# Kernel optimization log

Measured on AMD Instinct MI355X. Metric: run time of the kernel, lower is better.

## Reference

```python
import jax, jax.numpy as jnp
import numpy as np
import math

D_MODEL = 1024
D_STATE = 16
D_CONV = 4
EXPAND = 2
D_INNER = EXPAND * D_MODEL  # 2048
DT_RANK = 64
B_SZ = 2
L_SEQ = 1024


def setup_inputs() -> dict:
    key = jax.random.key(0)
    ks = jax.random.split(key, 10)
    x = jax.random.normal(ks[0], (B_SZ, L_SEQ, D_MODEL), dtype=jnp.float32)
    in_proj_w = jax.random.normal(ks[1], (2 * D_INNER, D_MODEL), dtype=jnp.float32) * (1.0 / math.sqrt(D_MODEL))
    conv_w = jax.random.normal(ks[2], (D_INNER, 1, D_CONV), dtype=jnp.float32) * (1.0 / math.sqrt(D_CONV))
    conv_b = jax.random.normal(ks[3], (D_INNER,), dtype=jnp.float32) * 0.01
    x_proj_w = jax.random.normal(ks[4], (DT_RANK + 2 * D_STATE, D_INNER), dtype=jnp.float32) * (1.0 / math.sqrt(D_INNER))
    dt_init_std = DT_RANK ** (-0.5)
    dt_proj_w = jax.random.uniform(ks[5], (D_INNER, DT_RANK), dtype=jnp.float32, minval=-dt_init_std, maxval=dt_init_std)
    dt = jnp.exp(jax.random.uniform(ks[6], (D_INNER,), dtype=jnp.float32) * (math.log(0.1) - math.log(0.001)) + math.log(0.001))
    dt = jnp.clip(dt, 1e-4, None)
    dt_proj_b = dt + jnp.log(-jnp.expm1(-dt))
    A_log = jnp.log(jnp.tile(jnp.arange(1, D_STATE + 1, dtype=jnp.float32)[None, :], (D_INNER, 1)))
    D = jnp.ones((D_INNER,), dtype=jnp.float32)
    out_proj_w = jax.random.normal(ks[7], (D_MODEL, D_INNER), dtype=jnp.float32) * (1.0 / math.sqrt(D_INNER))
    return {"x": x, "in_proj_w": in_proj_w, "conv_w": conv_w, "conv_b": conv_b,
            "x_proj_w": x_proj_w, "dt_proj_w": dt_proj_w, "dt_proj_b": dt_proj_b,
            "A_log": A_log, "D": D, "out_proj_w": out_proj_w}


def _mamba_forward(x, in_proj_w, conv_w, conv_b, x_proj_w, dt_proj_w, dt_proj_b, A_log, D, out_proj_w):
    B, L, _ = x.shape
    # input projection -> x, z each [B, L, Di]
    xz = jnp.einsum('bld,ed->ble', x, in_proj_w)
    xs, z = jnp.split(xz, 2, axis=-1)
    # causal depthwise conv along L (torch pads K-1 both sides then trims -> left pad only)
    xc = jnp.transpose(xs, (0, 2, 1))  # [B, Di, L]
    xc = jax.lax.conv_general_dilated(
        xc, conv_w, window_strides=(1,), padding=[(D_CONV - 1, 0)],
        feature_group_count=D_INNER, dimension_numbers=('NCH', 'OIH', 'NCH'))
    xc = xc + conv_b[None, :, None]
    xs = jnp.transpose(xc, (0, 2, 1))  # [B, L, Di]
    xs = jax.nn.silu(xs)
    # SSM parameters
    A = -jnp.exp(A_log)  # [Di, N]
    dbc = jnp.einsum('bld,ed->ble', xs, x_proj_w)
    delta_r = dbc[..., :DT_RANK]
    Bm = dbc[..., DT_RANK:DT_RANK + D_STATE]       # [B, L, N]
    Cm = dbc[..., DT_RANK + D_STATE:]              # [B, L, N]
    delta = jnp.einsum('blr,dr->bld', delta_r, dt_proj_w)
    delta = jax.nn.softplus(delta + dt_proj_b)     # [B, L, Di]
    # selective scan: h_t = exp(delta*A)*h_{t-1} + delta*B*x
    dA = jnp.exp(delta[..., None] * A)                          # [B, L, Di, N]
    dBx = (delta * xs)[..., None] * Bm[:, :, None, :]           # [B, L, Di, N]
    dA_t = jnp.moveaxis(dA, 1, 0)    # [L, B, Di, N]
    dBx_t = jnp.moveaxis(dBx, 1, 0)
    C_t = jnp.moveaxis(Cm, 1, 0)     # [L, B, N]
    h0 = jnp.zeros((B, D_INNER, D_STATE), dtype=xs.dtype)

    def step(h, inp):
        da, bx, c = inp
        h = da * h + bx
        y = jnp.einsum('bdn,bn->bd', h, c)
        return h, y

    _, ys = jax.lax.scan(step, h0, (dA_t, dBx_t, C_t))
    y = jnp.moveaxis(ys, 0, 1)       # [B, L, Di]
    y = y + D * xs
    # gating and output projection
    out = y * jax.nn.silu(z)
    return jnp.einsum('bld,od->blo', out, out_proj_w)


def reference(x, in_proj_w, conv_w, conv_b, x_proj_w, dt_proj_w, dt_proj_b, A_log, D, out_proj_w):
    return _mamba_forward(x, in_proj_w, conv_w, conv_b, x_proj_w, dt_proj_w, dt_proj_b, A_log, D, out_proj_w)
```

## Files before the change

kernel.cpp:

```cpp
#include <hip/hip_runtime.h>
#include <hip/hip_bf16.h>

typedef __attribute__((ext_vector_type(8))) short short8;
typedef __attribute__((ext_vector_type(4))) float f32x4;
typedef __hip_bfloat16 bf16;

#define D_MODEL 1024
#define D_INNER 2048
#define DT_RANK 64
#define D_STATE 16
#define B_SZ 2
#define L_SEQ 1024
#define NSEG 64
#define SL 16

__device__ __forceinline__ float b2f(bf16 x){ return __bfloat162float(x); }
__device__ __forceinline__ bf16  f2b(float x){ return __float2bfloat16(x); }

__device__ __forceinline__ void cvt_store8(bf16* dst, const float* s){
  union { short8 v; bf16 e[8]; } u;
  #pragma unroll
  for (int i = 0; i < 8; i++) u.e[i] = f2b(s[i]);
  *(short8*)dst = u.v;
}

__device__ __forceinline__ void gl_lds16(const bf16* g, bf16* l){
  __builtin_amdgcn_global_load_lds((const __attribute__((address_space(1))) unsigned int*)g,
                                   (__attribute__((address_space(3))) unsigned int*)l, 16, 0, 0);
}

__global__ __launch_bounds__(256) void cvt5_k(const float* s0, bf16* d0, int c0,
                                              const float* s1, bf16* d1, int c1,
                                              const float* s2, bf16* d2, int c2,
                                              const float* s3, bf16* d3, int c3,
                                              const float* s4, bf16* d4, int c4)
{
  int i = blockIdx.x * 256 + threadIdx.x;
  const float* s; bf16* d; int off;
  if      (i < c0) { s = s0; d = d0; off = i; }
  else if (i < c1) { s = s1; d = d1; off = i - c0; }
  else if (i < c2) { s = s2; d = d2; off = i - c1; }
  else if (i < c3) { s = s3; d = d3; off = i - c2; }
  else if (i < c4) { s = s4; d = d4; off = i - c3; }
  else return;
  float b[8];
  *(float4*)&b[0] = *(const float4*)(s + (size_t)off * 8);
  *(float4*)&b[4] = *(const float4*)(s + (size_t)off * 8 + 4);
  cvt_store8(d + (size_t)off * 8, b);
}

template<int MODE, int JT>
__global__ __launch_bounds__(256) void gemm_glds(const bf16* __restrict__ A,
                                                 const bf16* __restrict__ B,
                                                 void* __restrict__ Cout,
                                                 const float* __restrict__ bias,
                                                 int M, int N, int K)
{
  constexpr int BN = JT * 32;
  constexpr int BI = BN / 64;
  __shared__ bf16 As[128 * 32];
  __shared__ bf16 Bs[BN * 32];
  const int bm = blockIdx.y * 128, bn = blockIdx.x * BN;
  const int tid  = threadIdx.x;
  const int lane = tid & 63, wave = tid >> 6;
  const int wm = (wave & 1) * 64, wn = (wave >> 1) * (JT * 16);
  const int r = lane & 15, q = lane >> 4;

  const bf16* asrc[2];
  #pragma unroll
  for (int i = 0; i < 2; i++) {
    int c = i * 256 + tid;
    asrc[i] = A + (size_t)(bm + (c >> 2)) * K + (c & 3) * 8;
  }
  const bf16* bsrc[BI];
  #pragma unroll
  for (int i = 0; i < BI; i++) {
    int c = i * 256 + tid;
    bsrc[i] = B + (size_t)(bn + (c >> 2)) * K + (c & 3) * 8;
  }

  f32x4 acc[4][JT];
  #pragma unroll
  for (int i = 0; i < 4; i++)
    #pragma unroll
    for (int j = 0; j < JT; j++) acc[i][j] = (f32x4){0.f,0.f,0.f,0.f};

  for (int k0 = 0; k0 < K; k0 += 32) {
    #pragma unroll
    for (int i = 0; i < 2; i++)
      gl_lds16(asrc[i] + k0, &As[(i * 256 + tid) * 8]);
    #pragma unroll
    for (int i = 0; i < BI; i++)
      gl_lds16(bsrc[i] + k0, &Bs[(i * 256 + tid) * 8]);
    __syncthreads();
    short8 af[4], bfr[JT];
    #pragma unroll
    for (int i = 0; i < 4; i++)  af[i]  = *(const short8*)&As[(wm + i*16 + r) * 32 + q*8];
    #pragma unroll
    for (int j = 0; j < JT; j++) bfr[j] = *(const short8*)&Bs[(wn + j*16 + r) * 32 + q*8];
    #pragma unroll
    for (int j = 0; j < JT; j++)
      #pragma unroll
      for (int i = 0; i < 4; i++)
        acc[i][j] = __builtin_amdgcn_mfma_f32_16x16x32_bf16(af[i], bfr[j], acc[i][j], 0, 0, 0);
    __syncthreads();
  }

  #pragma unroll
  for (int i = 0; i < 4; i++)
    #pragma unroll
    for (int j = 0; j < JT; j++)
      #pragma unroll
      for (int t = 0; t < 4; t++) {
        int row = bm + wm + i*16 + q*4 + t;
        int col = bn + wn + j*16 + r;
        float v = acc[i][j][t];
        if (MODE == 0) {
          ((float*)Cout)[(size_t)row * N + col] = v;
        } else if (MODE == 1) {
          float xv = v + bias[col];
          float sp = (xv > 20.f) ? xv : log1pf(__expf(xv));
          ((float*)Cout)[(size_t)row * N + col] = sp;
        } else {
          ((bf16*)Cout)[(size_t)row * N + col] = f2b(v);
        }
      }
}

__global__ __launch_bounds__(256) void gemm_xproj(const bf16* __restrict__ A,
                                                  const bf16* __restrict__ W,
                                                  float* __restrict__ dbc,
                                                  bf16* __restrict__ dr)
{
  const int K = D_INNER;
  const int lane = threadIdx.x & 63, wave = threadIdx.x >> 6;
  const int mt = blockIdx.y * 4 + wave;
  const int nt = blockIdx.x;
  const int r = lane & 15, q = lane >> 4;
  const bf16* pa = A + (size_t)(mt*16 + r) * K + q*8;
  const bf16* pb = W + (size_t)(nt*16 + r) * K + q*8;
  f32x4 a0 = {0.f,0.f,0.f,0.f}, a1 = a0, a2 = a0, a3 = a0;
  for (int k0 = 0; k0 < K; k0 += 128) {
    short8 x0 = *(const short8*)(pa + k0);
    short8 w0 = *(const short8*)(pb + k0);
    short8 x1 = *(const short8*)(pa + k0 + 32);
    short8 w1 = *(const short8*)(pb + k0 + 32);
    short8 x2 = *(const short8*)(pa + k0 + 64);
    short8 w2 = *(const short8*)(pb + k0 + 64);
    short8 x3 = *(const short8*)(pa + k0 + 96);
    short8 w3 = *(const short8*)(pb + k0 + 96);
    a0 = __builtin_amdgcn_mfma_f32_16x16x32_bf16(x0, w0, a0, 0, 0, 0);
    a1 = __builtin_amdgcn_mfma_f32_16x16x32_bf16(x1, w1, a1, 0, 0, 0);
    a2 = __builtin_amdgcn_mfma_f32_16x16x32_bf16(x2, w2, a2, 0, 0, 0);
    a3 = __builtin_amdgcn_mfma_f32_16x16x32_bf16(x3, w3, a3, 0, 0, 0);
  }
  f32x4 acc = (a0 + a1) + (a2 + a3);
  #pragma unroll
  for (int t = 0; t < 4; t++) {
    int row = mt*16 + q*4 + t;
    int col = nt*16 + r;
    dbc[(size_t)row * 96 + col] = acc[t];
    if (col < DT_RANK) dr[(size_t)row * DT_RANK + col] = f2b(acc[t]);
  }
}

__global__ __launch_bounds__(256) void conv_silu_k(const bf16* __restrict__ xz,
                                                   const float* __restrict__ cw,
                                                   const float* __restrict__ cb,
                                                   bf16* __restrict__ xs_b)
{
  int idx = blockIdx.x * 256 + threadIdx.x;
  int d  = idx & (D_INNER - 1);
  int bl = idx >> 11;
  int l  = bl & (L_SEQ - 1);
  float acc = cb[d];
  #pragma unroll
  for (int j = 0; j < 4; ++j) {
    int lp = l - 3 + j;
    if (lp >= 0) acc += cw[d*4 + j] * b2f(xz[(size_t)(bl - 3 + j) * (2*D_INNER) + d]);
  }
  float s = acc / (1.f + __expf(-acc));
  xs_b[idx] = f2b(s);
}

__global__ __launch_bounds__(256) void scan_pass1(const float* __restrict__ delta,
                                                  const bf16* __restrict__ xs,
                                                  const float* __restrict__ dbc,
                                                  const float* __restrict__ A_log,
                                                  float* __restrict__ hseg,
                                                  float* __restrict__ Stot)
{
  __shared__ float bcs[SL][32];
  const int d   = blockIdx.x * 256 + threadIdx.x;
  const int seg = blockIdx.y, b = blockIdx.z;
  for (int i = threadIdx.x; i < SL*32; i += 256) {
    int l = i >> 5, c = i & 31;
    bcs[l][c] = dbc[((size_t)b*L_SEQ + seg*SL + l)*96 + DT_RANK + c];
  }
  __syncthreads();
  float An[16], h[16];
  #pragma unroll
  for (int n = 0; n < 16; n++) { An[n] = -__expf(A_log[d*16 + n]); h[n] = 0.f; }
  float S = 0.f;
  for (int li = 0; li < SL; ++li) {
    size_t bl = (size_t)b * L_SEQ + seg*SL + li;
    float dv = delta[bl*D_INNER + d];
    float xv = b2f(xs[bl*D_INNER + d]);
    S += dv;
    float dx = dv * xv;
    #pragma unroll
    for (int n = 0; n < 16; n++)
      h[n] = __expf(dv * An[n]) * h[n] + dx * bcs[li][n];
  }
  float* hp = hseg + (((size_t)seg*B_SZ + b)*D_INNER + d) * 16;
  #pragma unroll
  for (int n = 0; n < 16; n++) hp[n] = h[n];
  Stot[((size_t)seg*B_SZ + b)*D_INNER + d] = S;
}

__global__ __launch_bounds__(256) void scan_combine(const float* __restrict__ Stot,
                                                    float* __restrict__ hseg,
                                                    const float* __restrict__ A_log)
{
  int idx = blockIdx.x * 256 + threadIdx.x;
  int n = idx & 15;
  int d = (idx >> 4) & (D_INNER - 1);
  int b = idx >> 15;
  float An = -__expf(A_log[d*16 + n]);
  float H = 0.f;
  for (int s = 0; s < NSEG; s++) {
    size_t base = ((size_t)s*B_SZ + b)*D_INNER + d;
    float St   = Stot[base];
    float hloc = hseg[base*16 + n];
    hseg[base*16 + n] = H;
    H = __expf(An*St)*H + hloc;
  }
}

__global__ __launch_bounds__(256) void scan_pass3(const float* __restrict__ delta,
                                                  const bf16* __restrict__ xs,
                                                  const float* __restrict__ dbc,
                                                  const float* __restrict__ A_log,
                                                  const float* __restrict__ hseg,
                                                  const bf16* __restrict__ xz,
                                                  const float* __restrict__ Dw,
                                                  bf16* __restrict__ outin)
{
  __shared__ float bcs[SL][32];
  const int d   = blockIdx.x * 256 + threadIdx.x;
  const int seg = blockIdx.y, b = blockIdx.z;
  for (int i = threadIdx.x; i < SL*32; i += 256) {
    int l = i >> 5, c = i & 31;
    bcs[l][c] = dbc[((size_t)b*L_SEQ + seg*SL + l)*96 + DT_RANK + c];
  }
  __syncthreads();
  float An[16], h[16];
  const float* hp = hseg + (((size_t)seg*B_SZ + b)*D_INNER + d) * 16;
  #pragma unroll
  for (int n = 0; n < 16; n++) { An[n] = -__expf(A_log[d*16 + n]); h[n] = hp[n]; }
  const float Dv = Dw[d];
  for (int li = 0; li < SL; ++li) {
    size_t bl = (size_t)b * L_SEQ + seg*SL + li;
    float dv = delta[bl*D_INNER + d];
    float xv = b2f(xs[bl*D_INNER + d]);
    float dx = dv * xv;
    float y = 0.f;
    #pragma unroll
    for (int n = 0; n < 16; n++) {
      h[n] = __expf(dv * An[n]) * h[n] + dx * bcs[li][n];
      y   += h[n] * bcs[li][16 + n];
    }
    y += Dv * xv;
    float z = b2f(xz[bl*(size_t)(2*D_INNER) + D_INNER + d]);
    float g = z / (1.f + __expf(-z));
    outin[bl*D_INNER + d] = f2b(y * g);
  }
}

extern "C" void kernel_launch(void* const* d_in, const int* in_sizes, int n_in,
                              void* d_out, int out_size, void* d_ws, size_t ws_size,
                              hipStream_t stream)
{
  const float* x      = (const float*)d_in[0];
  const float* in_w   = (const float*)d_in[1];
  const float* conv_w = (const float*)d_in[2];
  const float* conv_b = (const float*)d_in[3];
  const float* xp_w   = (const float*)d_in[4];
  const float* dt_w   = (const float*)d_in[5];
  const float* dt_b   = (const float*)d_in[6];
  const float* A_log  = (const float*)d_in[7];
  const float* Dw     = (const float*)d_in[8];
  const float* out_w  = (const float*)d_in[9];
  float* out = (float*)d_out;

  char* p = (char*)d_ws;
  bf16*  xz    = (bf16*)p;  p += (size_t)B_SZ*L_SEQ*2*D_INNER*2;
  bf16*  xs_b  = (bf16*)p;  p += (size_t)B_SZ*L_SEQ*D_INNER*2;
  float* dbc   = (float*)p; p += (size_t)B_SZ*L_SEQ*96*4;
  bf16*  dr    = (bf16*)p;  p += (size_t)B_SZ*L_SEQ*DT_RANK*2;
  float* delta = (float*)p; p += (size_t)B_SZ*L_SEQ*D_INNER*4;
  float* Stot  = (float*)p; p += (size_t)NSEG*B_SZ*D_INNER*4;
  bf16*  outin = (bf16*)p;  p += (size_t)B_SZ*L_SEQ*D_INNER*2;
  bf16*  xp_wb = (bf16*)p;  p += (size_t)(DT_RANK+2*D_STATE)*D_INNER*2;
  bf16*  dt_wb = (bf16*)p;  p += (size_t)D_INNER*DT_RANK*2;
  bf16*  ow_b  = (bf16*)p;  p += (size_t)D_MODEL*D_INNER*2;
  char* u = p;
  bf16*  xb    = (bf16*)u;
  bf16*  in_wb = (bf16*)(u + (size_t)B_SZ*L_SEQ*D_MODEL*2);
  float* hseg  = (float*)u;
  p += (size_t)NSEG*B_SZ*D_INNER*16*4;

  const int M = B_SZ * L_SEQ;

  cvt5_k<<<4256, 256, 0, stream>>>(x, xb, 262144,
                                   in_w, in_wb, 786432,
                                   xp_w, xp_wb, 811008,
                                   dt_w, dt_wb, 827392,
                                   out_w, ow_b, 1089536);
  gemm_glds<2,4><<<dim3(2*D_INNER/128, M/128), 256, 0, stream>>>(xb, in_wb, xz, nullptr, M, 2*D_INNER, D_MODEL);
  conv_silu_k<<<(M*D_INNER)/256, 256, 0, stream>>>(xz, conv_w, conv_b, xs_b);
  gemm_xproj<<<dim3(6, M/64), 256, 0, stream>>>(xs_b, xp_wb, dbc, dr);
  gemm_glds<1,4><<<dim3(D_INNER/128, M/128), 256, 0, stream>>>(dr, dt_wb, delta, dt_b, M, D_INNER, DT_RANK);
  scan_pass1<<<dim3(D_INNER/256, NSEG, B_SZ), 256, 0, stream>>>(delta, xs_b, dbc, A_log, hseg, Stot);
  scan_combine<<<(B_SZ*D_INNER*16)/256, 256, 0, stream>>>(Stot, hseg, A_log);
  scan_pass3<<<dim3(D_INNER/256, NSEG, B_SZ), 256, 0, stream>>>(delta, xs_b, dbc, A_log, hseg, xz, Dw, outin);
  gemm_glds<0,2><<<dim3(D_MODEL/64, M/128), 256, 0, stream>>>(outin, ow_b, out, nullptr, M, D_MODEL, D_INNER);
}
```

Measured before the change: 273.2 us.

## Fuse dt projection into scan passes, merge combine, swizzle GEMM tiles, vectorize conv

```diff
diff --git a/kernel.cpp b/kernel.cpp
--- a/kernel.cpp
+++ b/kernel.cpp
@@ -11,8 +11,8 @@
 #define D_STATE 16
 #define B_SZ 2
 #define L_SEQ 1024
-#define NSEG 64
-#define SL 16
+#define NSEG 32
+#define SL 32
 
 __device__ __forceinline__ float b2f(bf16 x){ return __bfloat162float(x); }
 __device__ __forceinline__ bf16  f2b(float x){ return __float2bfloat16(x); }
@@ -53,14 +53,19 @@
 __global__ __launch_bounds__(256) void gemm_glds(const bf16* __restrict__ A,
                                                  const bf16* __restrict__ B,
                                                  void* __restrict__ Cout,
-                                                 const float* __restrict__ bias,
                                                  int M, int N, int K)
 {
   constexpr int BN = JT * 32;
   constexpr int BI = BN / 64;
   __shared__ bf16 As[128 * 32];
   __shared__ bf16 Bs[BN * 32];
-  const int bm = blockIdx.y * 128, bn = blockIdx.x * BN;
+
+  const int gx = gridDim.x;
+  const int nwg = gx * gridDim.y;
+  const int flat = blockIdx.y * gx + blockIdx.x;
+  const int swz = (flat & 7) * (nwg >> 3) + (flat >> 3);
+  const int bm = (swz / gx) * 128, bn = (swz % gx) * BN;
+
   const int tid  = threadIdx.x;
   const int lane = tid & 63, wave = tid >> 6;
   const int wm = (wave & 1) * 64, wn = (wave >> 1) * (JT * 16);
@@ -115,22 +120,14 @@
         int row = bm + wm + i*16 + q*4 + t;
         int col = bn + wn + j*16 + r;
         float v = acc[i][j][t];
-        if (MODE == 0) {
-          ((float*)Cout)[(size_t)row * N + col] = v;
-        } else if (MODE == 1) {
-          float xv = v + bias[col];
-          float sp = (xv > 20.f) ? xv : log1pf(__expf(xv));
-          ((float*)Cout)[(size_t)row * N + col] = sp;
-        } else {
-          ((bf16*)Cout)[(size_t)row * N + col] = f2b(v);
-        }
+        if (MODE == 0) ((float*)Cout)[(size_t)row * N + col] = v;
+        else           ((bf16*)Cout)[(size_t)row * N + col] = f2b(v);
       }
 }
 
 __global__ __launch_bounds__(256) void gemm_xproj(const bf16* __restrict__ A,
                                                   const bf16* __restrict__ W,
-                                                  float* __restrict__ dbc,
-                                                  bf16* __restrict__ dr)
+                                                  float* __restrict__ dbc)
 {
   const int K = D_INNER;
   const int lane = threadIdx.x & 63, wave = threadIdx.x >> 6;
@@ -160,7 +157,6 @@
     int row = mt*16 + q*4 + t;
     int col = nt*16 + r;
     dbc[(size_t)row * 96 + col] = acc[t];
-    if (col < DT_RANK) dr[(size_t)row * DT_RANK + col] = f2b(acc[t]);
   }
 }
 
@@ -170,41 +166,101 @@
                                                    bf16* __restrict__ xs_b)
 {
   int idx = blockIdx.x * 256 + threadIdx.x;
-  int d  = idx & (D_INNER - 1);
-  int bl = idx >> 11;
+  int dg = idx & (D_INNER/8 - 1);
+  int bl = idx >> 8;
   int l  = bl & (L_SEQ - 1);
-  float acc = cb[d];
+  int d0 = dg * 8;
+  const float4* cw4 = (const float4*)cw;
+  float4 w[8];
+  #pragma unroll
+  for (int i = 0; i < 8; i++) w[i] = cw4[d0 + i];
+  float acc[8];
+  #pragma unroll
+  for (int i = 0; i < 8; i++) acc[i] = cb[d0 + i];
   #pragma unroll
   for (int j = 0; j < 4; ++j) {
     int lp = l - 3 + j;
-    if (lp >= 0) acc += cw[d*4 + j] * b2f(xz[(size_t)(bl - 3 + j) * (2*D_INNER) + d]);
-  }
-  float s = acc / (1.f + __expf(-acc));
-  xs_b[idx] = f2b(s);
-}
-
-__global__ __launch_bounds__(256) void scan_pass1(const float* __restrict__ delta,
-                                                  const bf16* __restrict__ xs,
-                                                  const float* __restrict__ dbc,
-                                                  const float* __restrict__ A_log,
-                                                  float* __restrict__ hseg,
-                                                  float* __restrict__ Stot)
-{
+    if (lp >= 0) {
+      short8 v = *(const short8*)(xz + (size_t)(bl - 3 + j) * (2*D_INNER) + d0);
+      #pragma unroll
+      for (int i = 0; i < 8; i++)
+        acc[i] += ((const float*)&w[i])[j] * b2f(((const bf16*)&v)[i]);
+    }
+  }
+  float o[8];
+  #pragma unroll
+  for (int i = 0; i < 8; i++) o[i] = acc[i] / (1.f + __expf(-acc[i]));
+  cvt_store8(xs_b + (size_t)idx * 8, o);
+}
+
+__device__ __forceinline__ void stage_dbc(const float* __restrict__ dbc,
+                                          int b, int seg, int tid,
+                                          float (*drs)[64], float (*bcs)[32])
+{
+  for (int i = tid; i < SL*96; i += 256) {
+    int l = i / 96, c = i - l*96;
+    float v = dbc[((size_t)b*L_SEQ + seg*SL + l)*96 + c];
+    if (c < DT_RANK) drs[l][c] = v;
+    else             bcs[l][c - DT_RANK] = v;
+  }
+}
+
+#define LOAD_DTW(wf, dtw, d)                                            \
+  {                                                                     \
+    const short8* wp_ = (const short8*)((dtw) + (size_t)(d) * 64);      \
+    short8 wv_[8];                                                      \
+    _Pragma("unroll")                                                   \
+    for (int kk = 0; kk < 8; kk++) wv_[kk] = wp_[kk];                   \
+    _Pragma("unroll")                                                   \
+    for (int kk = 0; kk < 8; kk++)                                      \
+      _Pragma("unroll")                                                 \
+      for (int e = 0; e < 8; e++)                                       \
+        wf[kk*8 + e] = b2f(((const bf16*)&wv_[kk])[e]);                 \
+  }
+
+__device__ __forceinline__ float delta_dot(const float (*drs)[64], int li,
+                                           const float* wf, float bias)
+{
+  float a0 = 0.f, a1 = 0.f, a2 = 0.f, a3 = 0.f;
+  const float* dl = &drs[li][0];
+  #pragma unroll
+  for (int kk = 0; kk < 16; kk++) {
+    float4 v = *(const float4*)(dl + kk*4);
+    a0 += v.x * wf[kk*4 + 0];
+    a1 += v.y * wf[kk*4 + 1];
+    a2 += v.z * wf[kk*4 + 2];
+    a3 += v.w * wf[kk*4 + 3];
+  }
+  float xv = bias + (a0 + a1) + (a2 + a3);
+  return (xv > 20.f) ? xv : log1pf(__expf(xv));
+}
+
+__global__ __launch_bounds__(256) void scan_p1(const float* __restrict__ dbc,
+                                               const bf16* __restrict__ dtw,
+                                               const float* __restrict__ dt_b,
+                                               const bf16* __restrict__ xs,
+                                               const float* __restrict__ A_log,
+                                               float* __restrict__ hseg,
+                                               float* __restrict__ Stot)
+{
+  __shared__ float drs[SL][64];
   __shared__ float bcs[SL][32];
-  const int d   = blockIdx.x * 256 + threadIdx.x;
+  const int tid = threadIdx.x;
+  const int d   = blockIdx.x * 256 + tid;
   const int seg = blockIdx.y, b = blockIdx.z;
-  for (int i = threadIdx.x; i < SL*32; i += 256) {
-    int l = i >> 5, c = i & 31;
-    bcs[l][c] = dbc[((size_t)b*L_SEQ + seg*SL + l)*96 + DT_RANK + c];
-  }
+  stage_dbc(dbc, b, seg, tid, drs, bcs);
   __syncthreads();
+
+  float wf[64];
+  LOAD_DTW(wf, dtw, d);
+  const float bias = dt_b[d];
   float An[16], h[16];
   #pragma unroll
   for (int n = 0; n < 16; n++) { An[n] = -__expf(A_log[d*16 + n]); h[n] = 0.f; }
   float S = 0.f;
   for (int li = 0; li < SL; ++li) {
     size_t bl = (size_t)b * L_SEQ + seg*SL + li;
-    float dv = delta[bl*D_INNER + d];
+    float dv = delta_dot(drs, li, wf, bias);
     float xv = b2f(xs[bl*D_INNER + d]);
     S += dv;
     float dx = dv * xv;
@@ -218,50 +274,47 @@
   Stot[((size_t)seg*B_SZ + b)*D_INNER + d] = S;
 }
 
-__global__ __launch_bounds__(256) void scan_combine(const float* __restrict__ Stot,
-                                                    float* __restrict__ hseg,
-                                                    const float* __restrict__ A_log)
-{
-  int idx = blockIdx.x * 256 + threadIdx.x;
-  int n = idx & 15;
-  int d = (idx >> 4) & (D_INNER - 1);
-  int b = idx >> 15;
-  float An = -__expf(A_log[d*16 + n]);
-  float H = 0.f;
-  for (int s = 0; s < NSEG; s++) {
+__global__ __launch_bounds__(256) void scan_p23(const float* __restrict__ dbc,
+                                                const bf16* __restrict__ dtw,
+                                                const float* __restrict__ dt_b,
+                                                const bf16* __restrict__ xs,
+                                                const float* __restrict__ A_log,
+                                                const float* __restrict__ hseg,
+                                                const float* __restrict__ Stot,
+                                                const bf16* __restrict__ xz,
+                                                const float* __restrict__ Dw,
+                                                bf16* __restrict__ outin)
+{
+  __shared__ float drs[SL][64];
+  __shared__ float bcs[SL][32];
+  const int tid = threadIdx.x;
+  const int d   = blockIdx.x * 256 + tid;
+  const int seg = blockIdx.y, b = blockIdx.z;
+  stage_dbc(dbc, b, seg, tid, drs, bcs);
+
+  float An[16], h[16];
+  #pragma unroll
+  for (int n = 0; n < 16; n++) { An[n] = -__expf(A_log[d*16 + n]); h[n] = 0.f; }
+  for (int s = 0; s < seg; ++s) {
     size_t base = ((size_t)s*B_SZ + b)*D_INNER + d;
-    float St   = Stot[base];
-    float hloc = hseg[base*16 + n];
-    hseg[base*16 + n] = H;
-    H = __expf(An*St)*H + hloc;
-  }
-}
-
-__global__ __launch_bounds__(256) void scan_pass3(const float* __restrict__ delta,
-                                                  const bf16* __restrict__ xs,
-                                                  const float* __restrict__ dbc,
-                                                  const float* __restrict__ A_log,
-                                                  const float* __restrict__ hseg,
-                                                  const bf16* __restrict__ xz,
-                                                  const float* __restrict__ Dw,
-                                                  bf16* __restrict__ outin)
-{
-  __shared__ float bcs[SL][32];
-  const int d   = blockIdx.x * 256 + threadIdx.x;
-  const int seg = blockIdx.y, b = blockIdx.z;
-  for (int i = threadIdx.x; i < SL*32; i += 256) {
-    int l = i >> 5, c = i & 31;
-    bcs[l][c] = dbc[((size_t)b*L_SEQ + seg*SL + l)*96 + DT_RANK + c];
+    float St = Stot[base];
+    const float4* hp4 = (const float4*)(hseg + base*16);
+    float4 e0 = hp4[0], e1 = hp4[1], e2 = hp4[2], e3 = hp4[3];
+    float he[16] = {e0.x,e0.y,e0.z,e0.w, e1.x,e1.y,e1.z,e1.w,
+                    e2.x,e2.y,e2.z,e2.w, e3.x,e3.y,e3.z,e3.w};
+    #pragma unroll
+    for (int n = 0; n < 16; n++)
+      h[n] = __expf(An[n]*St) * h[n] + he[n];
   }
   __syncthreads();
-  float An[16], h[16];
-  const float* hp = hseg + (((size_t)seg*B_SZ + b)*D_INNER + d) * 16;
-  #pragma unroll
-  for (int n = 0; n < 16; n++) { An[n] = -__expf(A_log[d*16 + n]); h[n] = hp[n]; }
+
+  float wf[64];
+  LOAD_DTW(wf, dtw, d);
+  const float bias = dt_b[d];
   const float Dv = Dw[d];
   for (int li = 0; li < SL; ++li) {
     size_t bl = (size_t)b * L_SEQ + seg*SL + li;
-    float dv = delta[bl*D_INNER + d];
+    float dv = delta_dot(drs, li, wf, bias);
     float xv = b2f(xs[bl*D_INNER + d]);
     float dx = dv * xv;
     float y = 0.f;
@@ -297,8 +350,6 @@
   bf16*  xz    = (bf16*)p;  p += (size_t)B_SZ*L_SEQ*2*D_INNER*2;
   bf16*  xs_b  = (bf16*)p;  p += (size_t)B_SZ*L_SEQ*D_INNER*2;
   float* dbc   = (float*)p; p += (size_t)B_SZ*L_SEQ*96*4;
-  bf16*  dr    = (bf16*)p;  p += (size_t)B_SZ*L_SEQ*DT_RANK*2;
-  float* delta = (float*)p; p += (size_t)B_SZ*L_SEQ*D_INNER*4;
   float* Stot  = (float*)p; p += (size_t)NSEG*B_SZ*D_INNER*4;
   bf16*  outin = (bf16*)p;  p += (size_t)B_SZ*L_SEQ*D_INNER*2;
   bf16*  xp_wb = (bf16*)p;  p += (size_t)(DT_RANK+2*D_STATE)*D_INNER*2;
@@ -308,7 +359,7 @@
   bf16*  xb    = (bf16*)u;
   bf16*  in_wb = (bf16*)(u + (size_t)B_SZ*L_SEQ*D_MODEL*2);
   float* hseg  = (float*)u;
-  p += (size_t)NSEG*B_SZ*D_INNER*16*4;
+  p += (size_t)B_SZ*L_SEQ*(D_MODEL + 2*D_INNER)*2;
 
   const int M = B_SZ * L_SEQ;
 
@@ -317,12 +368,10 @@
                                    xp_w, xp_wb, 811008,
                                    dt_w, dt_wb, 827392,
                                    out_w, ow_b, 1089536);
-  gemm_glds<2,4><<<dim3(2*D_INNER/128, M/128), 256, 0, stream>>>(xb, in_wb, xz, nullptr, M, 2*D_INNER, D_MODEL);
-  conv_silu_k<<<(M*D_INNER)/256, 256, 0, stream>>>(xz, conv_w, conv_b, xs_b);
-  gemm_xproj<<<dim3(6, M/64), 256, 0, stream>>>(xs_b, xp_wb, dbc, dr);
-  gemm_glds<1,4><<<dim3(D_INNER/128, M/128), 256, 0, stream>>>(dr, dt_wb, delta, dt_b, M, D_INNER, DT_RANK);
-  scan_pass1<<<dim3(D_INNER/256, NSEG, B_SZ), 256, 0, stream>>>(delta, xs_b, dbc, A_log, hseg, Stot);
-  scan_combine<<<(B_SZ*D_INNER*16)/256, 256, 0, stream>>>(Stot, hseg, A_log);
-  scan_pass3<<<dim3(D_INNER/256, NSEG, B_SZ), 256, 0, stream>>>(delta, xs_b, dbc, A_log, hseg, xz, Dw, outin);
-  gemm_glds<0,2><<<dim3(D_MODEL/64, M/128), 256, 0, stream>>>(outin, ow_b, out, nullptr, M, D_MODEL, D_INNER);
-}
+  gemm_glds<2,2><<<dim3(2*D_INNER/64, M/128), 256, 0, stream>>>(xb, in_wb, xz, M, 2*D_INNER, D_MODEL);
+  conv_silu_k<<<(M*D_INNER/8)/256, 256, 0, stream>>>(xz, conv_w, conv_b, xs_b);
+  gemm_xproj<<<dim3(6, M/64), 256, 0, stream>>>(xs_b, xp_wb, dbc);
+  scan_p1<<<dim3(D_INNER/256, NSEG, B_SZ), 256, 0, stream>>>(dbc, dt_wb, dt_b, xs_b, A_log, hseg, Stot);
+  scan_p23<<<dim3(D_INNER/256, NSEG, B_SZ), 256, 0, stream>>>(dbc, dt_wb, dt_b, xs_b, A_log, hseg, Stot, xz, Dw, outin);
+  gemm_glds<0,2><<<dim3(D_MODEL/64, M/128), 256, 0, stream>>>(outin, ow_b, out, M, D_MODEL, D_INNER);
+}
```

New measurement: 299.3 us. +9.6%, slower.
